# Kernel tuning notes

Measured on AMD Instinct MI355X. Metric: run time of the kernel, lower is better.

Reference implementation:

```python
import jax, jax.numpy as jnp
import numpy as np

B, TT, TA, H = 2, 128, 512, 1024
EPS = 1e-5


def _conv1d(x, w, b, pad):
    # x: [B, C_in, T], w: [C_out, C_in, K] -> [B, C_out, T]
    y = jax.lax.conv_general_dilated(x, w, window_strides=(1,), padding=[(pad, pad)],
                                     dimension_numbers=('NCH', 'OIH', 'NCH'))
    return y + b[None, :, None]


def _groupnorm1(x, g, b):
    # GroupNorm(num_groups=1): normalize over (C, T) per sample. x: [B, C, T]
    mu = jnp.mean(x, axis=(1, 2), keepdims=True)
    var = jnp.var(x, axis=(1, 2), keepdims=True)
    xn = (x - mu) * jax.lax.rsqrt(var + EPS)
    return xn * g[None, :, None] + b[None, :, None]


def setup_inputs() -> dict:
    key = jax.random.key(0)
    ks = jax.random.split(key, 16)
    s = 0.02
    return {
        'text_hidden': jax.random.normal(ks[0], (B, TT, H), jnp.float32),
        'audio_hidden': jax.random.normal(ks[1], (B, TA, H), jnp.float32),
        # alignment_proj: Linear(2H, H) -> ReLU -> Linear(H, 1)
        'a_w1': jax.random.normal(ks[2], (2 * H, H), jnp.float32) * s,
        'a_b1': jnp.zeros((H,), jnp.float32),
        'a_w2': jax.random.normal(ks[3], (H, 1), jnp.float32) * s,
        'a_b2': jnp.zeros((1,), jnp.float32),
        # duration_predictor: Conv1d(H,H,3) ReLU GN(1,H) Conv1d(H,H,3) ReLU GN(1,H) Conv1d(H,1,1)
        'd_w1': jax.random.normal(ks[4], (H, H, 3), jnp.float32) * s,
        'd_b1': jnp.zeros((H,), jnp.float32),
        'gn1_g': jnp.ones((H,), jnp.float32),
        'gn1_b': jnp.zeros((H,), jnp.float32),
        'd_w2': jax.random.normal(ks[5], (H, H, 3), jnp.float32) * s,
        'd_b2': jnp.zeros((H,), jnp.float32),
        'gn2_g': jnp.ones((H,), jnp.float32),
        'gn2_b': jnp.zeros((H,), jnp.float32),
        'd_w3': jax.random.normal(ks[6], (1, H, 1), jnp.float32) * s,
        'd_b3': jnp.zeros((1,), jnp.float32),
    }


def reference(text_hidden, audio_hidden, a_w1, a_b1, a_w2, a_b2,
              d_w1, d_b1, gn1_g, gn1_b, d_w2, d_b2, gn2_g, gn2_b, d_w3, d_b3):
    # ---- predict_durations ----
    x = jnp.swapaxes(text_hidden, 1, 2)                      # [B, H, TT]
    x = _groupnorm1(jax.nn.relu(_conv1d(x, d_w1, d_b1, 1)), gn1_g, gn1_b)
    x = _groupnorm1(jax.nn.relu(_conv1d(x, d_w2, d_b2, 1)), gn2_g, gn2_b)
    x = _conv1d(x, d_w3, d_b3, 0)                            # [B, 1, TT]
    durations = jax.nn.softplus(x[:, 0, :])                  # [B, TT]

    # ---- soft_mas (temperature = 1.0) ----
    # Linear on concat([text, audio]) == text @ W1[:H] + audio @ W1[H:] + b1
    t_part = jnp.einsum('bth,hd->btd', text_hidden, a_w1[:H])    # [B, TT, H]
    a_part = jnp.einsum('bah,hd->bad', audio_hidden, a_w1[H:])   # [B, TA, H]
    hid = jax.nn.relu(t_part[:, :, None, :] + a_part[:, None, :, :] + a_b1)  # [B,TT,TA,H]
    logits = jnp.einsum('btad,do->bta', hid, a_w2) + a_b2[0]     # [B, TT, TA]

    pos = jnp.arange(TA, dtype=logits.dtype)                     # audio positions j
    expected = jnp.arange(TT, dtype=logits.dtype) * (TA / TT)    # expected pos per text i
    monotonic_bias = -0.1 * jnp.abs(pos[None, :] - expected[:, None])  # [TT, TA]
    logits = logits + monotonic_bias[None, :, :]

    alignment = jax.nn.softmax(logits, axis=-1)
    return alignment, durations
```

## Files before the change

### kernel.cpp

```cpp
#include <hip/hip_runtime.h>
#include <hip/hip_bf16.h>


typedef __bf16 bf16_t;
typedef __bf16 bf16x8 __attribute__((ext_vector_type(8)));
typedef __bf16 bf16x4 __attribute__((ext_vector_type(4)));
typedef float  f32x4  __attribute__((ext_vector_type(4)));
typedef _Float16 f16_t;
typedef _Float16 f16x2 __attribute__((ext_vector_type(2)));
typedef _Float16 f16x4 __attribute__((ext_vector_type(4)));

#define EPSV 1e-5f

#define OFF_TEXTBF   0u
#define OFF_AUDIOBF  524288u
#define OFF_W1TOP    2621440u
#define OFF_W1BOT    4718592u
#define OFF_WC1      6815744u
#define OFF_WC2      13107200u
#define OFF_TP       19398656u
#define OFF_W2F      19922944u
#define OFF_APT      20447232u
#define OFF_XP0      22544384u
#define OFF_XP1      23076864u
#define OFF_Y2       23609344u
#define OFF_BST1     24133632u
#define OFF_BST2     24137728u
#define OFF_LP       24141824u
#define OFF_SG       26238976u
#define OFF_SB       26251264u
#define OFF_SGF      26263552u
#define OFF_SBF      26267648u

__global__ __launch_bounds__(256) void prep_k(
    const float* __restrict__ text, const float* __restrict__ audio,
    const float* __restrict__ w1,
    const float* __restrict__ w1c, const float* __restrict__ w2c,
    const float* __restrict__ w2,
    const float* __restrict__ g1, const float* __restrict__ b1g,
    bf16_t* __restrict__ text_bf, bf16_t* __restrict__ xp0,
    bf16_t* __restrict__ audio_bf,
    bf16_t* __restrict__ topT, bf16_t* __restrict__ botT,
    bf16_t* __restrict__ wc1, bf16_t* __restrict__ wc2,
    bf16_t* __restrict__ xp1, f16_t* __restrict__ w2f,
    float* __restrict__ Sg, float* __restrict__ Sb,
    float* __restrict__ SgF, float* __restrict__ SbF)
{
    __shared__ float tile[32][33];
    const int bid = blockIdx.x;
    if (bid < 1280) {
        const int e = (bid * 256 + threadIdx.x) * 4;
        if (e < 262144) {
            float4 v = *(const float4*)&text[e];
            bf16x4 o; o[0] = (bf16_t)v.x; o[1] = (bf16_t)v.y; o[2] = (bf16_t)v.z; o[3] = (bf16_t)v.w;
            *(bf16x4*)&text_bf[e] = o;
            const int bt = e >> 10, h = e & 1023;
            const int b = bt >> 7, t = bt & 127;
            *(bf16x4*)&xp0[(size_t)(b * 130 + 1 + t) * 1024 + h] = o;
        } else {
            const int ea = e - 262144;
            float4 v = *(const float4*)&audio[ea];
            bf16x4 o; o[0] = (bf16_t)v.x; o[1] = (bf16_t)v.y; o[2] = (bf16_t)v.z; o[3] = (bf16_t)v.w;
            *(bf16x4*)&audio_bf[ea] = o;
        }
    } else if (bid < 3328) {
        const int b2 = bid - 1280;
        const int bx = b2 & 31, by = b2 >> 5;
        const int tx = threadIdx.x & 31, ty = threadIdx.x >> 5;
        #pragma unroll
        for (int j = 0; j < 4; ++j)
            tile[ty + j * 8][tx] = w1[(size_t)(by * 32 + ty + j * 8) * 1024 + bx * 32 + tx];
        __syncthreads();
        bf16_t* out = (by < 32) ? topT : botT;
        const int hbase = (by & 31) * 32;
        #pragma unroll
        for (int j = 0; j < 4; ++j) {
            const int d = bx * 32 + ty + j * 8;
            out[(size_t)d * 1024 + hbase + tx] = (bf16_t)tile[tx][ty + j * 8];
        }
    } else if (bid < 5376) {
        int b2 = bid - 3328;
        const int is2 = (b2 >= 1024) ? 1 : 0;
        const float* w = is2 ? w2c : w1c;
        bf16_t* wc = is2 ? wc2 : wc1;
        b2 &= 1023;
        const int o = b2, i4 = threadIdx.x;
        const float* src = w + (size_t)o * 3072 + i4 * 12;
        float4 v0 = *(const float4*)&src[0];
        float4 v1 = *(const float4*)&src[4];
        float4 v2 = *(const float4*)&src[8];
        const float f[12] = {v0.x, v0.y, v0.z, v0.w, v1.x, v1.y, v1.z, v1.w, v2.x, v2.y, v2.z, v2.w};
        float g4[4] = {1.f, 1.f, 1.f, 1.f}, bb4[4] = {0.f, 0.f, 0.f, 0.f};
        if (is2) {
            float4 gv = *(const float4*)&g1[i4 * 4];
            float4 bv = *(const float4*)&b1g[i4 * 4];
            g4[0] = gv.x; g4[1] = gv.y; g4[2] = gv.z; g4[3] = gv.w;
            bb4[0] = bv.x; bb4[1] = bv.y; bb4[2] = bv.z; bb4[3] = bv.w;
        }
        float sgr[3] = {0.f, 0.f, 0.f}, sbr[3] = {0.f, 0.f, 0.f};
        #pragma unroll
        for (int r = 0; r < 3; ++r) {
            bf16x4 o4;
            #pragma unroll
            for (int j = 0; j < 4; ++j) {
                const float wv = f[j * 3 + r];
                const float ws = wv * g4[j];
                sgr[r] += ws;
                sbr[r] += wv * bb4[j];
                o4[j] = (bf16_t)(is2 ? ws : wv);
            }
            *(bf16x4*)&wc[(size_t)r * 1048576 + (size_t)o * 1024 + i4 * 4] = o4;
        }
        if (is2) {
            #pragma unroll
            for (int off = 32; off > 0; off >>= 1) {
                #pragma unroll
                for (int r = 0; r < 3; ++r) {
                    sgr[r] += __shfl_xor(sgr[r], off);
                    sbr[r] += __shfl_xor(sbr[r], off);
                }
            }
            float* red = &tile[0][0];
            const int wid = threadIdx.x >> 6, lane = threadIdx.x & 63;
            if (lane == 0) {
                #pragma unroll
                for (int r = 0; r < 3; ++r) {
                    red[wid * 6 + r] = sgr[r];
                    red[wid * 6 + 3 + r] = sbr[r];
                }
            }
            __syncthreads();
            if (threadIdx.x < 6) {
                const float v = red[threadIdx.x] + red[6 + threadIdx.x]
                              + red[12 + threadIdx.x] + red[18 + threadIdx.x];
                if (threadIdx.x < 3) Sg[o * 3 + threadIdx.x] = v;
                else                 Sb[o * 3 + threadIdx.x - 3] = v;
                red[24 + threadIdx.x] = v;
            }
            __syncthreads();
            if (threadIdx.x == 0)      SgF[o] = red[24] + red[25] + red[26];
            else if (threadIdx.x == 1) SbF[o] = red[27] + red[28] + red[29];
        }
    } else {
        const int tid = threadIdx.x;
        const int rowmap[4] = {0, 129, 130, 259};
        const int f = tid * 16;
        const int r = f >> 10, w = f & 1023;
        bf16x8 z8 = (bf16x8)(bf16_t)0.0f;
        bf16_t* p0 = xp0 + (size_t)rowmap[r] * 1024 + w;
        bf16_t* p1 = xp1 + (size_t)rowmap[r] * 1024 + w;
        *(bf16x8*)p0 = z8; *(bf16x8*)(p0 + 8) = z8;
        *(bf16x8*)p1 = z8; *(bf16x8*)(p1 + 8) = z8;
        float4 wv = *(const float4*)&w2[tid * 4];
        f16x4 wo; wo[0] = (f16_t)wv.x; wo[1] = (f16_t)wv.y; wo[2] = (f16_t)wv.z; wo[3] = (f16_t)wv.w;
        *(f16x4*)&w2f[tid * 4] = wo;
    }
}

__device__ __forceinline__ float wave_red_add(float v) {
    #pragma unroll
    for (int off = 32; off > 0; off >>= 1) v += __shfl_xor(v, off);
    return v;
}

__device__ __forceinline__ void conv_wave_partial(
    const bf16_t* __restrict__ Wc, const bf16_t* __restrict__ xp,
    int m0, int b, int tbase, int w, int l, f32x4& acc0, f32x4& acc1)
{
    const int lm = l & 15, lk = (l >> 4) * 8;
    const int koff = w * 128;
    const bf16_t* aq = Wc + (size_t)(m0 + lm) * 1024 + koff + lk;
    const bf16_t* bq = xp + (size_t)(b * 130 + tbase + lm) * 1024 + koff + lk;
    #pragma unroll
    for (int s = 0; s < 2; ++s) {
        bf16x8 ra[6], rb0[6], rb1[6];
        #pragma unroll
        for (int j = 0; j < 6; ++j) {
            const int idx = s * 6 + j;
            const int rr = idx >> 2, cc = idx & 3;
            const bf16_t* pa = aq + (size_t)rr * 1048576 + cc * 32;
            const bf16_t* pb = bq + (size_t)rr * 1024 + cc * 32;
            ra[j]  = *(const bf16x8*)pa;
            rb0[j] = *(const bf16x8*)pb;
            rb1[j] = *(const bf16x8*)(pb + 16384);
        }
        #pragma unroll
        for (int j = 0; j < 6; ++j) {
            acc0 = __builtin_amdgcn_mfma_f32_16x16x32_bf16(ra[j], rb0[j], acc0, 0, 0, 0);
            acc1 = __builtin_amdgcn_mfma_f32_16x16x32_bf16(ra[j], rb1[j], acc1, 0, 0, 0);
        }
    }
}

__global__ __launch_bounds__(512) void p2_k(
    const bf16_t* __restrict__ wc1, const bf16_t* __restrict__ xp0,
    const float* __restrict__ d_b1, bf16_t* __restrict__ xp1,
    float* __restrict__ bstat1,
    const bf16_t* __restrict__ text_bf, const bf16_t* __restrict__ w1topT,
    const float* __restrict__ a_b1, f16_t* __restrict__ tp,
    const bf16_t* __restrict__ audio_bf, const bf16_t* __restrict__ w1botT,
    f16_t* __restrict__ apT4)
{
    __shared__ float smem[8448];
    __shared__ float sred[8], sredq[8];
    const int bid = blockIdx.x;
    const int tid = threadIdx.x;
    const int w = tid >> 6, l = tid & 63;
    const int lm = l & 15, lh = l >> 4, lk = lh * 8;
    if (bid < 512) {
        const int bx = bid >> 6, by = bid & 63;
        const int bt0 = bx * 32, m0 = by * 16;
        const int b = bt0 >> 7, tbase = bt0 & 127;
        f32x4 acc0 = (f32x4)(0.0f), acc1 = (f32x4)(0.0f);
        conv_wave_partial(wc1, xp0, m0, b, tbase, w, l, acc0, acc1);
        float* sl = smem + w * 528;
        #pragma unroll
        for (int r = 0; r < 4; ++r) {
            sl[(lh * 4 + r) * 33 + lm] = acc0[r];
            sl[(lh * 4 + r) * 33 + 16 + lm] = acc1[r];
        }
        __syncthreads();
        const int mm = tid >> 5, nn = tid & 31;
        float v = 0.f;
        #pragma unroll
        for (int ww = 0; ww < 8; ++ww) v += smem[ww * 528 + mm * 33 + nn];
        v = fmaxf(v + d_b1[m0 + mm], 0.f);
        float s = wave_red_add(v), q = wave_red_add(v * v);
        if (l == 0) { sred[w] = s; sredq[w] = q; }
        xp1[(size_t)(b * 130 + 1 + tbase + nn) * 1024 + m0 + mm] = (bf16_t)v;
        __syncthreads();
        if (tid == 0) {
            float ts = 0.f, tq = 0.f;
            #pragma unroll
            for (int ww = 0; ww < 8; ++ww) { ts += sred[ww]; tq += sredq[ww]; }
            bstat1[bid * 2] = ts; bstat1[bid * 2 + 1] = tq;
        }
    } else {
        const bf16_t *At, *Bm;
        int d0, r0, is_tp;
        if (bid < 768) {
            const int unit = bid - 512;
            d0 = (unit & 31) * 32; r0 = (unit >> 5) * 32;
            At = w1topT; Bm = text_bf; is_tp = 1;
        } else {
            const int unit = bid - 768;
            d0 = (unit & 31) * 32; r0 = (unit >> 5) * 32;
            At = w1botT; Bm = audio_bf; is_tp = 0;
        }
        const int koff = w * 128;
        const bf16_t* Ap = At + (size_t)(d0 + lm) * 1024 + koff + lk;
        const bf16_t* Bp = Bm + (size_t)(r0 + lm) * 1024 + koff + lk;
        bf16x8 qa0[4], qa1[4], qb0[4], qb1[4];
        #pragma unroll
        for (int cc = 0; cc < 4; ++cc) {
            qa0[cc] = *(const bf16x8*)(Ap + cc * 32);
            qa1[cc] = *(const bf16x8*)(Ap + 16384 + cc * 32);
            qb0[cc] = *(const bf16x8*)(Bp + cc * 32);
            qb1[cc] = *(const bf16x8*)(Bp + 16384 + cc * 32);
        }
        f32x4 acc[2][2];
        #pragma unroll
        for (int mt = 0; mt < 2; ++mt)
            #pragma unroll
            for (int nt = 0; nt < 2; ++nt) acc[mt][nt] = (f32x4)(0.0f);
        #pragma unroll
        for (int cc = 0; cc < 4; ++cc) {
            acc[0][0] = __builtin_amdgcn_mfma_f32_16x16x32_bf16(qa0[cc], qb0[cc], acc[0][0], 0, 0, 0);
            acc[0][1] = __builtin_amdgcn_mfma_f32_16x16x32_bf16(qa0[cc], qb1[cc], acc[0][1], 0, 0, 0);
            acc[1][0] = __builtin_amdgcn_mfma_f32_16x16x32_bf16(qa1[cc], qb0[cc], acc[1][0], 0, 0, 0);
            acc[1][1] = __builtin_amdgcn_mfma_f32_16x16x32_bf16(qa1[cc], qb1[cc], acc[1][1], 0, 0, 0);
        }
        float* sl = smem + w * 1056;
        #pragma unroll
        for (int mt = 0; mt < 2; ++mt)
            #pragma unroll
            for (int nt = 0; nt < 2; ++nt)
                #pragma unroll
                for (int r = 0; r < 4; ++r)
                    sl[(mt * 16 + lh * 4 + r) * 33 + nt * 16 + lm] = acc[mt][nt][r];
        __syncthreads();
        const int m = tid >> 4, n2 = (tid & 15) * 2;
        float v0 = 0.f, v1 = 0.f;
        #pragma unroll
        for (int ww = 0; ww < 8; ++ww) {
            v0 += smem[ww * 1056 + m * 33 + n2];
            v1 += smem[ww * 1056 + m * 33 + n2 + 1];
        }
        if (is_tp) {
            const float bb = a_b1[d0 + m];
            tp[(size_t)(r0 + n2) * 1024 + d0 + m] = (f16_t)(v0 + bb);
            tp[(size_t)(r0 + n2 + 1) * 1024 + d0 + m] = (f16_t)(v1 + bb);
        } else {
            const int h = d0 + m, hq = h >> 2, hr = h & 3;
            const int a0 = r0 + n2;
            const int bbk = a0 >> 9, al = a0 & 511;
            apT4[((size_t)hq * 1024 + bbk * 512 + al) * 4 + hr] = (f16_t)v0;
            apT4[((size_t)hq * 1024 + bbk * 512 + al + 1) * 4 + hr] = (f16_t)v1;
        }
    }
}

__device__ __forceinline__ void reduce_bstat(
    const float* __restrict__ bstat, int b, int tid,
    float* sr, float* sq, float& mu, float& rsig)
{
    const int lane = tid & 63, wid = tid >> 6;
    float s = 0.f, q = 0.f;
    if (tid < 256) {
        float2 v = ((const float2*)bstat)[b * 256 + tid];
        s = v.x; q = v.y;
    }
    #pragma unroll
    for (int off = 32; off > 0; off >>= 1) {
        s += __shfl_xor(s, off);
        q += __shfl_xor(q, off);
    }
    if (lane == 0) { sr[wid] = s; sq[wid] = q; }
    __syncthreads();
    float ts = 0.f, tq = 0.f;
    #pragma unroll
    for (int i = 0; i < 8; ++i) { ts += sr[i]; tq += sq[i]; }
    const float cnt = 131072.f;
    mu = ts / cnt;
    const float var = tq / cnt - mu * mu;
    rsig = rsqrtf(var + EPSV);
}

__device__ __forceinline__ float dot2_acc(f16x2 x, f16x2 w, float acc) {
#if __has_builtin(__builtin_amdgcn_fdot2)
    return __builtin_amdgcn_fdot2(x, w, acc, false);
#else
    return acc + (float)x[0] * (float)w[0] + (float)x[1] * (float)w[1];
#endif
}

__global__ __launch_bounds__(512) void p3_k(
    const bf16_t* __restrict__ wc2, const bf16_t* __restrict__ xp1,
    const float* __restrict__ d_b2, bf16_t* __restrict__ y2,
    float* __restrict__ bstat2, const float* __restrict__ bstat1,
    const float* __restrict__ SgF, const float* __restrict__ SbF,
    const float* __restrict__ Sg3, const float* __restrict__ Sb3,
    const f16_t* __restrict__ tp, const f16_t* __restrict__ apT4,
    const f16_t* __restrict__ w2f, float* __restrict__ lp)
{
    __shared__ float smem[4224];
    __shared__ float sred[8], sredq[8], sr[8], sq[8];
    const int bid = blockIdx.x;
    const int tid = threadIdx.x;
    if (bid < 512) {
        const int w = tid >> 6, l = tid & 63;
        const int lm = l & 15, lh = l >> 4;
        const int bx = bid >> 6, by = bid & 63;
        const int bt0 = bx * 32, m0 = by * 16;
        const int b = bt0 >> 7, tbase = bt0 & 127;
        f32x4 acc0 = (f32x4)(0.0f), acc1 = (f32x4)(0.0f);
        conv_wave_partial(wc2, xp1, m0, b, tbase, w, l, acc0, acc1);
        float* sl = smem + w * 528;
        #pragma unroll
        for (int r = 0; r < 4; ++r) {
            sl[(lh * 4 + r) * 33 + lm] = acc0[r];
            sl[(lh * 4 + r) * 33 + 16 + lm] = acc1[r];
        }
        __syncthreads();
        const int mm = tid >> 5, nn = tid & 31;
        float vraw = 0.f;
        #pragma unroll
        for (int ww = 0; ww < 8; ++ww) vraw += smem[ww * 528 + mm * 33 + nn];
        float mu, rsig;
        reduce_bstat(bstat1, b, tid, sr, sq, mu, rsig);
        const int o = m0 + mm, tloc = tbase + nn;
        float sg = SgF[o], sb = SbF[o];
        if (tloc == 0)   { sg -= Sg3[o * 3];     sb -= Sb3[o * 3]; }
        if (tloc == 127) { sg -= Sg3[o * 3 + 2]; sb -= Sb3[o * 3 + 2]; }
        float v = fmaxf(rsig * vraw + sb - mu * rsig * sg + d_b2[o], 0.f);
        float s = wave_red_add(v), q = wave_red_add(v * v);
        if ((tid & 63) == 0) { sred[tid >> 6] = s; sredq[tid >> 6] = q; }
        y2[(size_t)(b * 128 + tloc) * 1024 + o] = (bf16_t)v;
        __syncthreads();
        if (tid == 0) {
            float ts = 0.f, tq = 0.f;
            #pragma unroll
            for (int ww = 0; ww < 8; ++ww) { ts += sred[ww]; tq += sredq[ww]; }
            bstat2[bid * 2] = ts; bstat2[bid * 2 + 1] = tq;
        }
    } else {
        const int lb = bid - 512;
        const int hc = lb >> 6, btp = lb & 63;
        const int bt0 = btp * 4;
        const int b = bt0 >> 7;
        const int a = tid;
        const f16_t* tpr = tp + (size_t)bt0 * 1024 + hc * 256;
        const f16_t* w2r = w2f + hc * 256;
        const f16_t* apc = apT4 + ((size_t)(hc * 64) * 1024 + b * 512 + a) * 4;
        float acc[4] = {0.f, 0.f, 0.f, 0.f};
        const f16x2 zero = (f16x2)(f16_t)0.0f;
#define L_A0(i) (*(const f16x4*)(apc + (size_t)(2 * (i)) * 4096))
#define L_A1(i) (*(const f16x4*)(apc + (size_t)(2 * (i) + 1) * 4096))
        constexpr int PF = 4;
        f16x4 pa[PF], pb[PF];
        #pragma unroll
        for (int i = 0; i < PF; ++i) { pa[i] = L_A0(i); pb[i] = L_A1(i); }
        #pragma unroll
        for (int i = 0; i < 32; ++i) {
            const int sl = i % PF;
            const int hq = 2 * i;
            f16x4 a0 = pa[sl], a1 = pb[sl];
            f16x4 w0 = *(const f16x4*)&w2r[hq * 4];
            f16x4 w1 = *(const f16x4*)&w2r[hq * 4 + 4];
            #pragma unroll
            for (int r = 0; r < 4; ++r) {
                f16x4 t0 = *(const f16x4*)&tpr[r * 1024 + hq * 4];
                f16x4 t1 = *(const f16x4*)&tpr[r * 1024 + hq * 4 + 4];
                f16x2 p;
                p = __builtin_elementwise_max((f16x2){t0[0] + a0[0], t0[1] + a0[1]}, zero);
                acc[r] = dot2_acc(p, (f16x2){w0[0], w0[1]}, acc[r]);
                p = __builtin_elementwise_max((f16x2){t0[2] + a0[2], t0[3] + a0[3]}, zero);
                acc[r] = dot2_acc(p, (f16x2){w0[2], w0[3]}, acc[r]);
                p = __builtin_elementwise_max((f16x2){t1[0] + a1[0], t1[1] + a1[1]}, zero);
                acc[r] = dot2_acc(p, (f16x2){w1[0], w1[1]}, acc[r]);
                p = __builtin_elementwise_max((f16x2){t1[2] + a1[2], t1[3] + a1[3]}, zero);
                acc[r] = dot2_acc(p, (f16x2){w1[2], w1[3]}, acc[r]);
            }
            const int nx = i + PF;
            if (nx < 32) { pa[sl] = L_A0(nx); pb[sl] = L_A1(nx); }
        }
#undef L_A0
#undef L_A1
        float* dst = lp + (size_t)(hc * 256 + bt0) * 512 + a;
        #pragma unroll
        for (int r = 0; r < 4; ++r) dst[(size_t)r * 512] = acc[r];
    }
}

__global__ __launch_bounds__(512) void combine_k(
    const float* __restrict__ lp, const float* __restrict__ b2,
    const bf16_t* __restrict__ y2, const float* __restrict__ bstat2,
    const float* __restrict__ g, const float* __restrict__ bet,
    const float* __restrict__ w3, const float* __restrict__ b3,
    float* __restrict__ out)
{
    __shared__ float redm[8], redsum[8];
    const int bid = blockIdx.x;
    const int tid = threadIdx.x;
    if (bid < 256) {
        const int bt = bid, t = bt & 127;
        const int a = tid;
        const int lane = a & 63, wid = a >> 6;
        const size_t base = (size_t)bt * 512 + a;
        float v = lp[base] + lp[131072 + base] + lp[262144 + base] + lp[393216 + base];
        v += b2[0] - 0.1f * fabsf((float)a - 4.0f * (float)t);
        float m = v;
        #pragma unroll
        for (int off = 32; off > 0; off >>= 1) m = fmaxf(m, __shfl_xor(m, off));
        if (lane == 0) redm[wid] = m;
        __syncthreads();
        float M = redm[0];
        #pragma unroll
        for (int i = 1; i < 8; ++i) M = fmaxf(M, redm[i]);
        const float e = expf(v - M);
        float s = e;
        #pragma unroll
        for (int off = 32; off > 0; off >>= 1) s += __shfl_xor(s, off);
        if (lane == 0) redsum[wid] = s;
        __syncthreads();
        float S = redsum[0];
        #pragma unroll
        for (int i = 1; i < 8; ++i) S += redsum[i];
        out[(size_t)bt * 512 + a] = e * (1.0f / S);
    } else {
        const int cb = bid - 256;
        const int b = (cb * 8) >> 7;
        float mu, rsig;
        reduce_bstat(bstat2, b, tid, redm, redsum, mu, rsig);
        const int lane = tid & 63, w = tid >> 6;
        const int bt = cb * 8 + w;
        const bf16_t* row = y2 + (size_t)bt * 1024 + lane * 16;
        float s1 = 0.f, s2 = 0.f, s3 = 0.f;
        #pragma unroll
        for (int c = 0; c < 2; ++c) {
            bf16x8 yv = *(const bf16x8*)(row + c * 8);
            #pragma unroll
            for (int j = 0; j < 8; ++j) {
                const int i = lane * 16 + c * 8 + j;
                const float gw = g[i] * w3[i];
                s1 += gw * (float)yv[j];
                s2 += gw;
                s3 += bet[i] * w3[i];
            }
        }
        #pragma unroll
        for (int off = 32; off > 0; off >>= 1) {
            s1 += __shfl_xor(s1, off);
            s2 += __shfl_xor(s2, off);
            s3 += __shfl_xor(s3, off);
        }
        if (lane == 0) {
            const float t = rsig * (s1 - mu * s2) + s3 + b3[0];
            out[131072 + bt] = fmaxf(t, 0.f) + log1pf(expf(-fabsf(t)));
        }
    }
}

extern "C" void kernel_launch(void* const* d_in, const int* in_sizes, int n_in,
                              void* d_out, int out_size, void* d_ws, size_t ws_size,
                              hipStream_t stream) {
    const float* text   = (const float*)d_in[0];
    const float* audio  = (const float*)d_in[1];
    const float* a_w1   = (const float*)d_in[2];
    const float* a_b1   = (const float*)d_in[3];
    const float* a_w2   = (const float*)d_in[4];
    const float* a_b2   = (const float*)d_in[5];
    const float* d_w1   = (const float*)d_in[6];
    const float* d_b1   = (const float*)d_in[7];
    const float* gn1_g  = (const float*)d_in[8];
    const float* gn1_b  = (const float*)d_in[9];
    const float* d_w2   = (const float*)d_in[10];
    const float* d_b2   = (const float*)d_in[11];
    const float* gn2_g  = (const float*)d_in[12];
    const float* gn2_b  = (const float*)d_in[13];
    const float* d_w3   = (const float*)d_in[14];
    const float* d_b3   = (const float*)d_in[15];

    char* ws = (char*)d_ws;
    float* outf = (float*)d_out;

    bf16_t* text_bf  = (bf16_t*)(ws + OFF_TEXTBF);
    bf16_t* audio_bf = (bf16_t*)(ws + OFF_AUDIOBF);
    bf16_t* w1topT   = (bf16_t*)(ws + OFF_W1TOP);
    bf16_t* w1botT   = (bf16_t*)(ws + OFF_W1BOT);
    bf16_t* wc1      = (bf16_t*)(ws + OFF_WC1);
    bf16_t* wc2      = (bf16_t*)(ws + OFF_WC2);
    f16_t*  tp       = (f16_t*) (ws + OFF_TP);
    f16_t*  w2f      = (f16_t*) (ws + OFF_W2F);
    f16_t*  apT4     = (f16_t*) (ws + OFF_APT);
    bf16_t* xp0      = (bf16_t*)(ws + OFF_XP0);
    bf16_t* xp1      = (bf16_t*)(ws + OFF_XP1);
    bf16_t* y2       = (bf16_t*)(ws + OFF_Y2);
    float*  bstat1   = (float*) (ws + OFF_BST1);
    float*  bstat2   = (float*) (ws + OFF_BST2);
    float*  lp       = (float*) (ws + OFF_LP);
    float*  Sg3     = (float*) (ws + OFF_SG);
    float*  Sb3     = (float*) (ws + OFF_SB);
    float*  SgFp    = (float*) (ws + OFF_SGF);
    float*  SbFp    = (float*) (ws + OFF_SBF);

    prep_k<<<dim3(5377), 256, 0, stream>>>(text, audio, a_w1, d_w1, d_w2, a_w2,
                                           gn1_g, gn1_b,
                                           text_bf, xp0, audio_bf, w1topT, w1botT,
                                           wc1, wc2, xp1, w2f, Sg3, Sb3,
                                           SgFp, SbFp);
    p2_k<<<dim3(1792), 512, 0, stream>>>(wc1, xp0, d_b1, xp1, bstat1,
                                         text_bf, w1topT, a_b1, tp,
                                         audio_bf, w1botT, apT4);
    p3_k<<<dim3(768), 512, 0, stream>>>(wc2, xp1, d_b2, y2, bstat2, bstat1,
                                        SgFp, SbFp, Sg3, Sb3, tp, apT4, w2f, lp);
    combine_k<<<dim3(288), 512, 0, stream>>>(lp, a_b2, y2, bstat2,
                                             gn2_g, gn2_b, d_w3, d_b3, outf);
}
```

Before: 179.5 us.

## Fuse four phase kernels into one cooperative persistent kernel with grid syncs

Turns the four separate kernel launches (prep, phase A, phase B, combine) into one cooperative kernel with 256 persistent blocks. The blocks loop over work units and use grid-wide barriers between phases. This aims to remove launch gaps and tail drain between kernels. In exchange it caps parallelism at 256 blocks, with each block running many units in sequence, and adds grid sync costs. A fallback to separate launches is kept in case the cooperative launch fails.

After: 294.8 us. +64.2%, slower.

```diff
diff --git a/kernel.cpp b/kernel.cpp
--- a/kernel.cpp
+++ b/kernel.cpp
@@ -1,5 +1,8 @@
 #include <hip/hip_runtime.h>
 #include <hip/hip_bf16.h>
+#include <hip/hip_cooperative_groups.h>
+
+namespace cg = cooperative_groups;
 
 
 typedef __bf16 bf16_t;
@@ -32,130 +35,14 @@
 #define OFF_SGF      26263552u
 #define OFF_SBF      26267648u
 
-__global__ __launch_bounds__(256) void prep_k(
-    const float* __restrict__ text, const float* __restrict__ audio,
-    const float* __restrict__ w1,
-    const float* __restrict__ w1c, const float* __restrict__ w2c,
-    const float* __restrict__ w2,
-    const float* __restrict__ g1, const float* __restrict__ b1g,
-    bf16_t* __restrict__ text_bf, bf16_t* __restrict__ xp0,
-    bf16_t* __restrict__ audio_bf,
-    bf16_t* __restrict__ topT, bf16_t* __restrict__ botT,
-    bf16_t* __restrict__ wc1, bf16_t* __restrict__ wc2,
-    bf16_t* __restrict__ xp1, f16_t* __restrict__ w2f,
-    float* __restrict__ Sg, float* __restrict__ Sb,
-    float* __restrict__ SgF, float* __restrict__ SbF)
-{
-    __shared__ float tile[32][33];
-    const int bid = blockIdx.x;
-    if (bid < 1280) {
-        const int e = (bid * 256 + threadIdx.x) * 4;
-        if (e < 262144) {
-            float4 v = *(const float4*)&text[e];
-            bf16x4 o; o[0] = (bf16_t)v.x; o[1] = (bf16_t)v.y; o[2] = (bf16_t)v.z; o[3] = (bf16_t)v.w;
-            *(bf16x4*)&text_bf[e] = o;
-            const int bt = e >> 10, h = e & 1023;
-            const int b = bt >> 7, t = bt & 127;
-            *(bf16x4*)&xp0[(size_t)(b * 130 + 1 + t) * 1024 + h] = o;
-        } else {
-            const int ea = e - 262144;
-            float4 v = *(const float4*)&audio[ea];
-            bf16x4 o; o[0] = (bf16_t)v.x; o[1] = (bf16_t)v.y; o[2] = (bf16_t)v.z; o[3] = (bf16_t)v.w;
-            *(bf16x4*)&audio_bf[ea] = o;
-        }
-    } else if (bid < 3328) {
-        const int b2 = bid - 1280;
-        const int bx = b2 & 31, by = b2 >> 5;
-        const int tx = threadIdx.x & 31, ty = threadIdx.x >> 5;
-        #pragma unroll
-        for (int j = 0; j < 4; ++j)
-            tile[ty + j * 8][tx] = w1[(size_t)(by * 32 + ty + j * 8) * 1024 + bx * 32 + tx];
-        __syncthreads();
-        bf16_t* out = (by < 32) ? topT : botT;
-        const int hbase = (by & 31) * 32;
-        #pragma unroll
-        for (int j = 0; j < 4; ++j) {
-            const int d = bx * 32 + ty + j * 8;
-            out[(size_t)d * 1024 + hbase + tx] = (bf16_t)tile[tx][ty + j * 8];
-        }
-    } else if (bid < 5376) {
-        int b2 = bid - 3328;
-        const int is2 = (b2 >= 1024) ? 1 : 0;
-        const float* w = is2 ? w2c : w1c;
-        bf16_t* wc = is2 ? wc2 : wc1;
-        b2 &= 1023;
-        const int o = b2, i4 = threadIdx.x;
-        const float* src = w + (size_t)o * 3072 + i4 * 12;
-        float4 v0 = *(const float4*)&src[0];
-        float4 v1 = *(const float4*)&src[4];
-        float4 v2 = *(const float4*)&src[8];
-        const float f[12] = {v0.x, v0.y, v0.z, v0.w, v1.x, v1.y, v1.z, v1.w, v2.x, v2.y, v2.z, v2.w};
-        float g4[4] = {1.f, 1.f, 1.f, 1.f}, bb4[4] = {0.f, 0.f, 0.f, 0.f};
-        if (is2) {
-            float4 gv = *(const float4*)&g1[i4 * 4];
-            float4 bv = *(const float4*)&b1g[i4 * 4];
-            g4[0] = gv.x; g4[1] = gv.y; g4[2] = gv.z; g4[3] = gv.w;
-            bb4[0] = bv.x; bb4[1] = bv.y; bb4[2] = bv.z; bb4[3] = bv.w;
-        }
-        float sgr[3] = {0.f, 0.f, 0.f}, sbr[3] = {0.f, 0.f, 0.f};
-        #pragma unroll
-        for (int r = 0; r < 3; ++r) {
-            bf16x4 o4;
-            #pragma unroll
-            for (int j = 0; j < 4; ++j) {
-                const float wv = f[j * 3 + r];
-                const float ws = wv * g4[j];
-                sgr[r] += ws;
-                sbr[r] += wv * bb4[j];
-                o4[j] = (bf16_t)(is2 ? ws : wv);
-            }
-            *(bf16x4*)&wc[(size_t)r * 1048576 + (size_t)o * 1024 + i4 * 4] = o4;
-        }
-        if (is2) {
-            #pragma unroll
-            for (int off = 32; off > 0; off >>= 1) {
-                #pragma unroll
-                for (int r = 0; r < 3; ++r) {
-                    sgr[r] += __shfl_xor(sgr[r], off);
-                    sbr[r] += __shfl_xor(sbr[r], off);
-                }
-            }
-            float* red = &tile[0][0];
-            const int wid = threadIdx.x >> 6, lane = threadIdx.x & 63;
-            if (lane == 0) {
-                #pragma unroll
-                for (int r = 0; r < 3; ++r) {
-                    red[wid * 6 + r] = sgr[r];
-                    red[wid * 6 + 3 + r] = sbr[r];
-                }
-            }
-            __syncthreads();
-            if (threadIdx.x < 6) {
-                const float v = red[threadIdx.x] + red[6 + threadIdx.x]
-                              + red[12 + threadIdx.x] + red[18 + threadIdx.x];
-                if (threadIdx.x < 3) Sg[o * 3 + threadIdx.x] = v;
-                else                 Sb[o * 3 + threadIdx.x - 3] = v;
-                red[24 + threadIdx.x] = v;
-            }
-            __syncthreads();
-            if (threadIdx.x == 0)      SgF[o] = red[24] + red[25] + red[26];
-            else if (threadIdx.x == 1) SbF[o] = red[27] + red[28] + red[29];
-        }
-    } else {
-        const int tid = threadIdx.x;
-        const int rowmap[4] = {0, 129, 130, 259};
-        const int f = tid * 16;
-        const int r = f >> 10, w = f & 1023;
-        bf16x8 z8 = (bf16x8)(bf16_t)0.0f;
-        bf16_t* p0 = xp0 + (size_t)rowmap[r] * 1024 + w;
-        bf16_t* p1 = xp1 + (size_t)rowmap[r] * 1024 + w;
-        *(bf16x8*)p0 = z8; *(bf16x8*)(p0 + 8) = z8;
-        *(bf16x8*)p1 = z8; *(bf16x8*)(p1 + 8) = z8;
-        float4 wv = *(const float4*)&w2[tid * 4];
-        f16x4 wo; wo[0] = (f16_t)wv.x; wo[1] = (f16_t)wv.y; wo[2] = (f16_t)wv.z; wo[3] = (f16_t)wv.w;
-        *(f16x4*)&w2f[tid * 4] = wo;
-    }
-}
+struct KP {
+    const float *text, *audio, *w1, *w1c, *w2c, *w2raw, *g1, *b1g;
+    const float *db1, *ab1, *db2, *ab2, *g2, *bet2, *w3, *b3;
+    bf16_t *text_bf, *audio_bf, *topT, *botT, *wc1, *wc2, *xp0, *xp1, *y2;
+    f16_t *tp, *w2f, *apT4;
+    float *bstat1, *bstat2, *lp, *Sg3, *Sb3, *SgF, *SbF;
+    float *out;
+};
 
 __device__ __forceinline__ float wave_red_add(float v) {
     #pragma unroll
@@ -188,114 +75,6 @@
         for (int j = 0; j < 6; ++j) {
             acc0 = __builtin_amdgcn_mfma_f32_16x16x32_bf16(ra[j], rb0[j], acc0, 0, 0, 0);
             acc1 = __builtin_amdgcn_mfma_f32_16x16x32_bf16(ra[j], rb1[j], acc1, 0, 0, 0);
-        }
-    }
-}
-
-__global__ __launch_bounds__(512) void p2_k(
-    const bf16_t* __restrict__ wc1, const bf16_t* __restrict__ xp0,
-    const float* __restrict__ d_b1, bf16_t* __restrict__ xp1,
-    float* __restrict__ bstat1,
-    const bf16_t* __restrict__ text_bf, const bf16_t* __restrict__ w1topT,
-    const float* __restrict__ a_b1, f16_t* __restrict__ tp,
-    const bf16_t* __restrict__ audio_bf, const bf16_t* __restrict__ w1botT,
-    f16_t* __restrict__ apT4)
-{
-    __shared__ float smem[8448];
-    __shared__ float sred[8], sredq[8];
-    const int bid = blockIdx.x;
-    const int tid = threadIdx.x;
-    const int w = tid >> 6, l = tid & 63;
-    const int lm = l & 15, lh = l >> 4, lk = lh * 8;
-    if (bid < 512) {
-        const int bx = bid >> 6, by = bid & 63;
-        const int bt0 = bx * 32, m0 = by * 16;
-        const int b = bt0 >> 7, tbase = bt0 & 127;
-        f32x4 acc0 = (f32x4)(0.0f), acc1 = (f32x4)(0.0f);
-        conv_wave_partial(wc1, xp0, m0, b, tbase, w, l, acc0, acc1);
-        float* sl = smem + w * 528;
-        #pragma unroll
-        for (int r = 0; r < 4; ++r) {
-            sl[(lh * 4 + r) * 33 + lm] = acc0[r];
-            sl[(lh * 4 + r) * 33 + 16 + lm] = acc1[r];
-        }
-        __syncthreads();
-        const int mm = tid >> 5, nn = tid & 31;
-        float v = 0.f;
-        #pragma unroll
-        for (int ww = 0; ww < 8; ++ww) v += smem[ww * 528 + mm * 33 + nn];
-        v = fmaxf(v + d_b1[m0 + mm], 0.f);
-        float s = wave_red_add(v), q = wave_red_add(v * v);
-        if (l == 0) { sred[w] = s; sredq[w] = q; }
-        xp1[(size_t)(b * 130 + 1 + tbase + nn) * 1024 + m0 + mm] = (bf16_t)v;
-        __syncthreads();
-        if (tid == 0) {
-            float ts = 0.f, tq = 0.f;
-            #pragma unroll
-            for (int ww = 0; ww < 8; ++ww) { ts += sred[ww]; tq += sredq[ww]; }
-            bstat1[bid * 2] = ts; bstat1[bid * 2 + 1] = tq;
-        }
-    } else {
-        const bf16_t *At, *Bm;
-        int d0, r0, is_tp;
-        if (bid < 768) {
-            const int unit = bid - 512;
-            d0 = (unit & 31) * 32; r0 = (unit >> 5) * 32;
-            At = w1topT; Bm = text_bf; is_tp = 1;
-        } else {
-            const int unit = bid - 768;
-            d0 = (unit & 31) * 32; r0 = (unit >> 5) * 32;
-            At = w1botT; Bm = audio_bf; is_tp = 0;
-        }
-        const int koff = w * 128;
-        const bf16_t* Ap = At + (size_t)(d0 + lm) * 1024 + koff + lk;
-        const bf16_t* Bp = Bm + (size_t)(r0 + lm) * 1024 + koff + lk;
-        bf16x8 qa0[4], qa1[4], qb0[4], qb1[4];
-        #pragma unroll
-        for (int cc = 0; cc < 4; ++cc) {
-            qa0[cc] = *(const bf16x8*)(Ap + cc * 32);
-            qa1[cc] = *(const bf16x8*)(Ap + 16384 + cc * 32);
-            qb0[cc] = *(const bf16x8*)(Bp + cc * 32);
-            qb1[cc] = *(const bf16x8*)(Bp + 16384 + cc * 32);
-        }
-        f32x4 acc[2][2];
-        #pragma unroll
-        for (int mt = 0; mt < 2; ++mt)
-            #pragma unroll
-            for (int nt = 0; nt < 2; ++nt) acc[mt][nt] = (f32x4)(0.0f);
-        #pragma unroll
-        for (int cc = 0; cc < 4; ++cc) {
-            acc[0][0] = __builtin_amdgcn_mfma_f32_16x16x32_bf16(qa0[cc], qb0[cc], acc[0][0], 0, 0, 0);
-            acc[0][1] = __builtin_amdgcn_mfma_f32_16x16x32_bf16(qa0[cc], qb1[cc], acc[0][1], 0, 0, 0);
-            acc[1][0] = __builtin_amdgcn_mfma_f32_16x16x32_bf16(qa1[cc], qb0[cc], acc[1][0], 0, 0, 0);
-            acc[1][1] = __builtin_amdgcn_mfma_f32_16x16x32_bf16(qa1[cc], qb1[cc], acc[1][1], 0, 0, 0);
-        }
-        float* sl = smem + w * 1056;
-        #pragma unroll
-        for (int mt = 0; mt < 2; ++mt)
-            #pragma unroll
-            for (int nt = 0; nt < 2; ++nt)
-                #pragma unroll
-                for (int r = 0; r < 4; ++r)
-                    sl[(mt * 16 + lh * 4 + r) * 33 + nt * 16 + lm] = acc[mt][nt][r];
-        __syncthreads();
-        const int m = tid >> 4, n2 = (tid & 15) * 2;
-        float v0 = 0.f, v1 = 0.f;
-        #pragma unroll
-        for (int ww = 0; ww < 8; ++ww) {
-            v0 += smem[ww * 1056 + m * 33 + n2];
-            v1 += smem[ww * 1056 + m * 33 + n2 + 1];
-        }
-        if (is_tp) {
-            const float bb = a_b1[d0 + m];
-            tp[(size_t)(r0 + n2) * 1024 + d0 + m] = (f16_t)(v0 + bb);
-            tp[(size_t)(r0 + n2 + 1) * 1024 + d0 + m] = (f16_t)(v1 + bb);
-        } else {
-            const int h = d0 + m, hq = h >> 2, hr = h & 3;
-            const int a0 = r0 + n2;
-            const int bbk = a0 >> 9, al = a0 & 511;
-            apT4[((size_t)hq * 1024 + bbk * 512 + al) * 4 + hr] = (f16_t)v0;
-            apT4[((size_t)hq * 1024 + bbk * 512 + al + 1) * 4 + hr] = (f16_t)v1;
         }
     }
 }
@@ -334,27 +113,126 @@
 #endif
 }
 
-__global__ __launch_bounds__(512) void p3_k(
-    const bf16_t* __restrict__ wc2, const bf16_t* __restrict__ xp1,
-    const float* __restrict__ d_b2, bf16_t* __restrict__ y2,
-    float* __restrict__ bstat2, const float* __restrict__ bstat1,
-    const float* __restrict__ SgF, const float* __restrict__ SbF,
-    const float* __restrict__ Sg3, const float* __restrict__ Sb3,
-    const f16_t* __restrict__ tp, const f16_t* __restrict__ apT4,
-    const f16_t* __restrict__ w2f, float* __restrict__ lp)
-{
-    __shared__ float smem[4224];
-    __shared__ float sred[8], sredq[8], sr[8], sq[8];
-    const int bid = blockIdx.x;
-    const int tid = threadIdx.x;
-    if (bid < 512) {
-        const int w = tid >> 6, l = tid & 63;
-        const int lm = l & 15, lh = l >> 4;
-        const int bx = bid >> 6, by = bid & 63;
+__device__ void prep_unit(int u, int t, float* tile, const KP& p)
+{
+    if (u < 1280) {
+        const int e = (u * 256 + t) * 4;
+        if (e < 262144) {
+            float4 v = *(const float4*)&p.text[e];
+            bf16x4 o; o[0] = (bf16_t)v.x; o[1] = (bf16_t)v.y; o[2] = (bf16_t)v.z; o[3] = (bf16_t)v.w;
+            *(bf16x4*)&p.text_bf[e] = o;
+            const int bt = e >> 10, h = e & 1023;
+            const int b = bt >> 7, tt = bt & 127;
+            *(bf16x4*)&p.xp0[(size_t)(b * 130 + 1 + tt) * 1024 + h] = o;
+        } else {
+            const int ea = e - 262144;
+            float4 v = *(const float4*)&p.audio[ea];
+            bf16x4 o; o[0] = (bf16_t)v.x; o[1] = (bf16_t)v.y; o[2] = (bf16_t)v.z; o[3] = (bf16_t)v.w;
+            *(bf16x4*)&p.audio_bf[ea] = o;
+        }
+    } else if (u < 3328) {
+        const int b2 = u - 1280;
+        const int bx = b2 & 31, by = b2 >> 5;
+        const int tx = t & 31, ty = t >> 5;
+        #pragma unroll
+        for (int j = 0; j < 4; ++j)
+            tile[(ty + j * 8) * 33 + tx] = p.w1[(size_t)(by * 32 + ty + j * 8) * 1024 + bx * 32 + tx];
+        __syncthreads();
+        bf16_t* out = (by < 32) ? p.topT : p.botT;
+        const int hbase = (by & 31) * 32;
+        #pragma unroll
+        for (int j = 0; j < 4; ++j) {
+            const int d = bx * 32 + ty + j * 8;
+            out[(size_t)d * 1024 + hbase + tx] = (bf16_t)tile[tx * 33 + ty + j * 8];
+        }
+    } else if (u < 5376) {
+        int b2 = u - 3328;
+        const int is2 = (b2 >= 1024) ? 1 : 0;
+        const float* wsrc = is2 ? p.w2c : p.w1c;
+        bf16_t* wc = is2 ? p.wc2 : p.wc1;
+        b2 &= 1023;
+        const int o = b2, i4 = t;
+        const float* src = wsrc + (size_t)o * 3072 + i4 * 12;
+        float4 v0 = *(const float4*)&src[0];
+        float4 v1 = *(const float4*)&src[4];
+        float4 v2 = *(const float4*)&src[8];
+        const float f[12] = {v0.x, v0.y, v0.z, v0.w, v1.x, v1.y, v1.z, v1.w, v2.x, v2.y, v2.z, v2.w};
+        float g4[4] = {1.f, 1.f, 1.f, 1.f}, bb4[4] = {0.f, 0.f, 0.f, 0.f};
+        if (is2) {
+            float4 gv = *(const float4*)&p.g1[i4 * 4];
+            float4 bv = *(const float4*)&p.b1g[i4 * 4];
+            g4[0] = gv.x; g4[1] = gv.y; g4[2] = gv.z; g4[3] = gv.w;
+            bb4[0] = bv.x; bb4[1] = bv.y; bb4[2] = bv.z; bb4[3] = bv.w;
+        }
+        float sgr[3] = {0.f, 0.f, 0.f}, sbr[3] = {0.f, 0.f, 0.f};
+        #pragma unroll
+        for (int r = 0; r < 3; ++r) {
+            bf16x4 o4;
+            #pragma unroll
+            for (int j = 0; j < 4; ++j) {
+                const float wv = f[j * 3 + r];
+                const float ws = wv * g4[j];
+                sgr[r] += ws;
+                sbr[r] += wv * bb4[j];
+                o4[j] = (bf16_t)(is2 ? ws : wv);
+            }
+            *(bf16x4*)&wc[(size_t)r * 1048576 + (size_t)o * 1024 + i4 * 4] = o4;
+        }
+        if (is2) {
+            #pragma unroll
+            for (int off = 32; off > 0; off >>= 1) {
+                #pragma unroll
+                for (int r = 0; r < 3; ++r) {
+                    sgr[r] += __shfl_xor(sgr[r], off);
+                    sbr[r] += __shfl_xor(sbr[r], off);
+                }
+            }
+            float* red = tile;
+            const int wid = t >> 6, lane = t & 63;
+            if (lane == 0) {
+                #pragma unroll
+                for (int r = 0; r < 3; ++r) {
+                    red[wid * 6 + r] = sgr[r];
+                    red[wid * 6 + 3 + r] = sbr[r];
+                }
+            }
+            __syncthreads();
+            if (t < 6) {
+                const float v = red[t] + red[6 + t] + red[12 + t] + red[18 + t];
+                if (t < 3) p.Sg3[o * 3 + t] = v;
+                else       p.Sb3[o * 3 + t - 3] = v;
+                red[24 + t] = v;
+            }
+            __syncthreads();
+            if (t == 0)      p.SgF[o] = red[24] + red[25] + red[26];
+            else if (t == 1) p.SbF[o] = red[27] + red[28] + red[29];
+        }
+    } else {
+        const int rowmap[4] = {0, 129, 130, 259};
+        const int f = t * 16;
+        const int r = f >> 10, ww = f & 1023;
+        bf16x8 z8 = (bf16x8)(bf16_t)0.0f;
+        bf16_t* p0 = p.xp0 + (size_t)rowmap[r] * 1024 + ww;
+        bf16_t* p1 = p.xp1 + (size_t)rowmap[r] * 1024 + ww;
+        *(bf16x8*)p0 = z8; *(bf16x8*)(p0 + 8) = z8;
+        *(bf16x8*)p1 = z8; *(bf16x8*)(p1 + 8) = z8;
+        float4 wv = *(const float4*)&p.w2raw[t * 4];
+        f16x4 wo; wo[0] = (f16_t)wv.x; wo[1] = (f16_t)wv.y; wo[2] = (f16_t)wv.z; wo[3] = (f16_t)wv.w;
+        *(f16x4*)&p.w2f[t * 4] = wo;
+    }
+}
+
+__device__ void phaseA_unit(int u, int tid, float* smem,
+                            float* sred, float* sredq, const KP& p)
+{
+    const int w = tid >> 6, l = tid & 63;
+    const int lm = l & 15, lh = l >> 4, lk = lh * 8;
+    if (u < 512) {
+        const int bx = u >> 6, by = u & 63;
         const int bt0 = bx * 32, m0 = by * 16;
         const int b = bt0 >> 7, tbase = bt0 & 127;
         f32x4 acc0 = (f32x4)(0.0f), acc1 = (f32x4)(0.0f);
-        conv_wave_partial(wc2, xp1, m0, b, tbase, w, l, acc0, acc1);
+        conv_wave_partial(p.wc1, p.xp0, m0, b, tbase, w, l, acc0, acc1);
         float* sl = smem + w * 528;
         #pragma unroll
         for (int r = 0; r < 4; ++r) {
@@ -363,35 +241,135 @@
         }
         __syncthreads();
         const int mm = tid >> 5, nn = tid & 31;
+        float v = 0.f;
+        #pragma unroll
+        for (int ww = 0; ww < 8; ++ww) v += smem[ww * 528 + mm * 33 + nn];
+        v = fmaxf(v + p.db1[m0 + mm], 0.f);
+        float s = wave_red_add(v), q = wave_red_add(v * v);
+        if (l == 0) { sred[w] = s; sredq[w] = q; }
+        p.xp1[(size_t)(b * 130 + 1 + tbase + nn) * 1024 + m0 + mm] = (bf16_t)v;
+        __syncthreads();
+        if (tid == 0) {
+            float ts = 0.f, tq = 0.f;
+            #pragma unroll
+            for (int ww = 0; ww < 8; ++ww) { ts += sred[ww]; tq += sredq[ww]; }
+            p.bstat1[u * 2] = ts; p.bstat1[u * 2 + 1] = tq;
+        }
+    } else {
+        const int is_tp = (u < 768) ? 1 : 0;
+        int d0, r0;
+        const bf16_t *At, *Bm;
+        if (is_tp) {
+            const int un = u - 512;
+            d0 = (un & 31) * 32; r0 = (un >> 5) * 32;
+            At = p.topT; Bm = p.text_bf;
+        } else {
+            const int un = u - 768;
+            d0 = (un & 31) * 32; r0 = (un >> 5) * 32;
+            At = p.botT; Bm = p.audio_bf;
+        }
+        const int koff = w * 128;
+        const bf16_t* Ap = At + (size_t)(d0 + lm) * 1024 + koff + lk;
+        const bf16_t* Bp = Bm + (size_t)(r0 + lm) * 1024 + koff + lk;
+        bf16x8 qa0[4], qa1[4], qb0[4], qb1[4];
+        #pragma unroll
+        for (int cc = 0; cc < 4; ++cc) {
+            qa0[cc] = *(const bf16x8*)(Ap + cc * 32);
+            qa1[cc] = *(const bf16x8*)(Ap + 16384 + cc * 32);
+            qb0[cc] = *(const bf16x8*)(Bp + cc * 32);
+            qb1[cc] = *(const bf16x8*)(Bp + 16384 + cc * 32);
+        }
+        f32x4 acc[2][2];
+        #pragma unroll
+        for (int mt = 0; mt < 2; ++mt)
+            #pragma unroll
+            for (int nt = 0; nt < 2; ++nt) acc[mt][nt] = (f32x4)(0.0f);
+        #pragma unroll
+        for (int cc = 0; cc < 4; ++cc) {
+            acc[0][0] = __builtin_amdgcn_mfma_f32_16x16x32_bf16(qa0[cc], qb0[cc], acc[0][0], 0, 0, 0);
+            acc[0][1] = __builtin_amdgcn_mfma_f32_16x16x32_bf16(qa0[cc], qb1[cc], acc[0][1], 0, 0, 0);
+            acc[1][0] = __builtin_amdgcn_mfma_f32_16x16x32_bf16(qa1[cc], qb0[cc], acc[1][0], 0, 0, 0);
+            acc[1][1] = __builtin_amdgcn_mfma_f32_16x16x32_bf16(qa1[cc], qb1[cc], acc[1][1], 0, 0, 0);
+        }
+        float* sl = smem + w * 1056;
+        #pragma unroll
+        for (int mt = 0; mt < 2; ++mt)
+            #pragma unroll
+            for (int nt = 0; nt < 2; ++nt)
+                #pragma unroll
+                for (int r = 0; r < 4; ++r)
+                    sl[(mt * 16 + lh * 4 + r) * 33 + nt * 16 + lm] = acc[mt][nt][r];
+        __syncthreads();
+        const int m = tid >> 4, n2 = (tid & 15) * 2;
+        float v0 = 0.f, v1 = 0.f;
+        #pragma unroll
+        for (int ww = 0; ww < 8; ++ww) {
+            v0 += smem[ww * 1056 + m * 33 + n2];
+            v1 += smem[ww * 1056 + m * 33 + n2 + 1];
+        }
+        if (is_tp) {
+            const float bb = p.ab1[d0 + m];
+            p.tp[(size_t)(r0 + n2) * 1024 + d0 + m] = (f16_t)(v0 + bb);
+            p.tp[(size_t)(r0 + n2 + 1) * 1024 + d0 + m] = (f16_t)(v1 + bb);
+        } else {
+            const int h = d0 + m, hq = h >> 2, hr = h & 3;
+            const int a0 = r0 + n2;
+            const int bbk = a0 >> 9, al = a0 & 511;
+            p.apT4[((size_t)hq * 1024 + bbk * 512 + al) * 4 + hr] = (f16_t)v0;
+            p.apT4[((size_t)hq * 1024 + bbk * 512 + al + 1) * 4 + hr] = (f16_t)v1;
+        }
+    }
+}
+
+__device__ void phaseB_unit(int u, int tid, float* smem,
+                            float* sred, float* sredq, float* sr8, float* sq8,
+                            const KP& p)
+{
+    if (u < 512) {
+        const int w = tid >> 6, l = tid & 63;
+        const int lm = l & 15, lh = l >> 4;
+        const int bx = u >> 6, by = u & 63;
+        const int bt0 = bx * 32, m0 = by * 16;
+        const int b = bt0 >> 7, tbase = bt0 & 127;
+        f32x4 acc0 = (f32x4)(0.0f), acc1 = (f32x4)(0.0f);
+        conv_wave_partial(p.wc2, p.xp1, m0, b, tbase, w, l, acc0, acc1);
+        float* sl = smem + w * 528;
+        #pragma unroll
+        for (int r = 0; r < 4; ++r) {
+            sl[(lh * 4 + r) * 33 + lm] = acc0[r];
+            sl[(lh * 4 + r) * 33 + 16 + lm] = acc1[r];
+        }
+        __syncthreads();
+        const int mm = tid >> 5, nn = tid & 31;
         float vraw = 0.f;
         #pragma unroll
         for (int ww = 0; ww < 8; ++ww) vraw += smem[ww * 528 + mm * 33 + nn];
         float mu, rsig;
-        reduce_bstat(bstat1, b, tid, sr, sq, mu, rsig);
+        reduce_bstat(p.bstat1, b, tid, sr8, sq8, mu, rsig);
         const int o = m0 + mm, tloc = tbase + nn;
-        float sg = SgF[o], sb = SbF[o];
-        if (tloc == 0)   { sg -= Sg3[o * 3];     sb -= Sb3[o * 3]; }
-        if (tloc == 127) { sg -= Sg3[o * 3 + 2]; sb -= Sb3[o * 3 + 2]; }
-        float v = fmaxf(rsig * vraw + sb - mu * rsig * sg + d_b2[o], 0.f);
+        float sg = p.SgF[o], sb = p.SbF[o];
+        if (tloc == 0)   { sg -= p.Sg3[o * 3];     sb -= p.Sb3[o * 3]; }
+        if (tloc == 127) { sg -= p.Sg3[o * 3 + 2]; sb -= p.Sb3[o * 3 + 2]; }
+        float v = fmaxf(rsig * vraw + sb - mu * rsig * sg + p.db2[o], 0.f);
         float s = wave_red_add(v), q = wave_red_add(v * v);
         if ((tid & 63) == 0) { sred[tid >> 6] = s; sredq[tid >> 6] = q; }
-        y2[(size_t)(b * 128 + tloc) * 1024 + o] = (bf16_t)v;
+        p.y2[(size_t)(b * 128 + tloc) * 1024 + o] = (bf16_t)v;
         __syncthreads();
         if (tid == 0) {
             float ts = 0.f, tq = 0.f;
             #pragma unroll
             for (int ww = 0; ww < 8; ++ww) { ts += sred[ww]; tq += sredq[ww]; }
-            bstat2[bid * 2] = ts; bstat2[bid * 2 + 1] = tq;
+            p.bstat2[u * 2] = ts; p.bstat2[u * 2 + 1] = tq;
         }
     } else {
-        const int lb = bid - 512;
+        const int lb = u - 512;
         const int hc = lb >> 6, btp = lb & 63;
         const int bt0 = btp * 4;
         const int b = bt0 >> 7;
         const int a = tid;
-        const f16_t* tpr = tp + (size_t)bt0 * 1024 + hc * 256;
-        const f16_t* w2r = w2f + hc * 256;
-        const f16_t* apc = apT4 + ((size_t)(hc * 64) * 1024 + b * 512 + a) * 4;
+        const f16_t* tpr = p.tp + (size_t)bt0 * 1024 + hc * 256;
+        const f16_t* w2r = p.w2f + hc * 256;
+        const f16_t* apc = p.apT4 + ((size_t)(hc * 64) * 1024 + b * 512 + a) * 4;
         float acc[4] = {0.f, 0.f, 0.f, 0.f};
         const f16x2 zero = (f16x2)(f16_t)0.0f;
 #define L_A0(i) (*(const f16x4*)(apc + (size_t)(2 * (i)) * 4096))
@@ -411,70 +389,64 @@
             for (int r = 0; r < 4; ++r) {
                 f16x4 t0 = *(const f16x4*)&tpr[r * 1024 + hq * 4];
                 f16x4 t1 = *(const f16x4*)&tpr[r * 1024 + hq * 4 + 4];
-                f16x2 p;
-                p = __builtin_elementwise_max((f16x2){t0[0] + a0[0], t0[1] + a0[1]}, zero);
-                acc[r] = dot2_acc(p, (f16x2){w0[0], w0[1]}, acc[r]);
-                p = __builtin_elementwise_max((f16x2){t0[2] + a0[2], t0[3] + a0[3]}, zero);
-                acc[r] = dot2_acc(p, (f16x2){w0[2], w0[3]}, acc[r]);
-                p = __builtin_elementwise_max((f16x2){t1[0] + a1[0], t1[1] + a1[1]}, zero);
-                acc[r] = dot2_acc(p, (f16x2){w1[0], w1[1]}, acc[r]);
-                p = __builtin_elementwise_max((f16x2){t1[2] + a1[2], t1[3] + a1[3]}, zero);
-                acc[r] = dot2_acc(p, (f16x2){w1[2], w1[3]}, acc[r]);
+                f16x2 pp;
+                pp = __builtin_elementwise_max((f16x2){t0[0] + a0[0], t0[1] + a0[1]}, zero);
+                acc[r] = dot2_acc(pp, (f16x2){w0[0], w0[1]}, acc[r]);
+                pp = __builtin_elementwise_max((f16x2){t0[2] + a0[2], t0[3] + a0[3]}, zero);
+                acc[r] = dot2_acc(pp, (f16x2){w0[2], w0[3]}, acc[r]);
+                pp = __builtin_elementwise_max((f16x2){t1[0] + a1[0], t1[1] + a1[1]}, zero);
+                acc[r] = dot2_acc(pp, (f16x2){w1[0], w1[1]}, acc[r]);
+                pp = __builtin_elementwise_max((f16x2){t1[2] + a1[2], t1[3] + a1[3]}, zero);
+                acc[r] = dot2_acc(pp, (f16x2){w1[2], w1[3]}, acc[r]);
             }
             const int nx = i + PF;
             if (nx < 32) { pa[sl] = L_A0(nx); pb[sl] = L_A1(nx); }
         }
 #undef L_A0
 #undef L_A1
-        float* dst = lp + (size_t)(hc * 256 + bt0) * 512 + a;
+        float* dst = p.lp + (size_t)(hc * 256 + bt0) * 512 + a;
         #pragma unroll
         for (int r = 0; r < 4; ++r) dst[(size_t)r * 512] = acc[r];
     }
 }
 
-__global__ __launch_bounds__(512) void combine_k(
-    const float* __restrict__ lp, const float* __restrict__ b2,
-    const bf16_t* __restrict__ y2, const float* __restrict__ bstat2,
-    const float* __restrict__ g, const float* __restrict__ bet,
-    const float* __restrict__ w3, const float* __restrict__ b3,
-    float* __restrict__ out)
-{
-    __shared__ float redm[8], redsum[8];
-    const int bid = blockIdx.x;
-    const int tid = threadIdx.x;
-    if (bid < 256) {
-        const int bt = bid, t = bt & 127;
+__device__ void phaseC_unit(int u, int tid,
+                            float* sred, float* sredq, float* sr8, float* sq8,
+                            const KP& p)
+{
+    if (u < 256) {
+        const int bt = u, t = bt & 127;
         const int a = tid;
         const int lane = a & 63, wid = a >> 6;
         const size_t base = (size_t)bt * 512 + a;
-        float v = lp[base] + lp[131072 + base] + lp[262144 + base] + lp[393216 + base];
-        v += b2[0] - 0.1f * fabsf((float)a - 4.0f * (float)t);
+        float v = p.lp[base] + p.lp[131072 + base] + p.lp[262144 + base] + p.lp[393216 + base];
+        v += p.ab2[0] - 0.1f * fabsf((float)a - 4.0f * (float)t);
         float m = v;
         #pragma unroll
         for (int off = 32; off > 0; off >>= 1) m = fmaxf(m, __shfl_xor(m, off));
-        if (lane == 0) redm[wid] = m;
-        __syncthreads();
-        float M = redm[0];
-        #pragma unroll
-        for (int i = 1; i < 8; ++i) M = fmaxf(M, redm[i]);
+        if (lane == 0) sred[wid] = m;
+        __syncthreads();
+        float M = sred[0];
+        #pragma unroll
+        for (int i = 1; i < 8; ++i) M = fmaxf(M, sred[i]);
         const float e = expf(v - M);
         float s = e;
         #pragma unroll
         for (int off = 32; off > 0; off >>= 1) s += __shfl_xor(s, off);
-        if (lane == 0) redsum[wid] = s;
-        __syncthreads();
-        float S = redsum[0];
-        #pragma unroll
-        for (int i = 1; i < 8; ++i) S += redsum[i];
-        out[(size_t)bt * 512 + a] = e * (1.0f / S);
+        if (lane == 0) sredq[wid] = s;
+        __syncthreads();
+        float S = sredq[0];
+        #pragma unroll
+        for (int i = 1; i < 8; ++i) S += sredq[i];
+        p.out[(size_t)bt * 512 + a] = e * (1.0f / S);
     } else {
-        const int cb = bid - 256;
+        const int cb = u - 256;
         const int b = (cb * 8) >> 7;
         float mu, rsig;
-        reduce_bstat(bstat2, b, tid, redm, redsum, mu, rsig);
-        const int lane = tid & 63, w = tid >> 6;
-        const int bt = cb * 8 + w;
-        const bf16_t* row = y2 + (size_t)bt * 1024 + lane * 16;
+        reduce_bstat(p.bstat2, b, tid, sr8, sq8, mu, rsig);
+        const int lane = tid & 63, ww = tid >> 6;
+        const int bt = cb * 8 + ww;
+        const bf16_t* row = p.y2 + (size_t)bt * 1024 + lane * 16;
         float s1 = 0.f, s2 = 0.f, s3 = 0.f;
         #pragma unroll
         for (int c = 0; c < 2; ++c) {
@@ -482,10 +454,10 @@
             #pragma unroll
             for (int j = 0; j < 8; ++j) {
                 const int i = lane * 16 + c * 8 + j;
-                const float gw = g[i] * w3[i];
+                const float gw = p.g2[i] * p.w3[i];
                 s1 += gw * (float)yv[j];
                 s2 += gw;
-                s3 += bet[i] * w3[i];
+                s3 += p.bet2[i] * p.w3[i];
             }
         }
         #pragma unroll
@@ -495,65 +467,109 @@
             s3 += __shfl_xor(s3, off);
         }
         if (lane == 0) {
-            const float t = rsig * (s1 - mu * s2) + s3 + b3[0];
-            out[131072 + bt] = fmaxf(t, 0.f) + log1pf(expf(-fabsf(t)));
-        }
-    }
+            const float t = rsig * (s1 - mu * s2) + s3 + p.b3[0];
+            p.out[131072 + bt] = fmaxf(t, 0.f) + log1pf(expf(-fabsf(t)));
+        }
+    }
+}
+
+__global__ __launch_bounds__(512, 2) void fused_k(KP p)
+{
+    cg::grid_group gg = cg::this_grid();
+    __shared__ float smem[8448];
+    __shared__ float sred[8], sredq[8], sr8[8], sq8[8];
+    const int gs = gridDim.x;
+    const int bid = blockIdx.x;
+    const int tid = threadIdx.x;
+
+    {
+        const int half = tid >> 8, t = tid & 255;
+        float* tile = smem + half * 1056;
+        for (int i = bid; i < 2689; i += gs) {
+            __syncthreads();
+            const int u = i * 2 + half;
+            if (u < 5377) prep_unit(u, t, tile, p);
+        }
+    }
+    gg.sync();
+    for (int u = bid; u < 1792; u += gs) { __syncthreads(); phaseA_unit(u, tid, smem, sred, sredq, p); }
+    gg.sync();
+    for (int u = bid; u < 768; u += gs) { __syncthreads(); phaseB_unit(u, tid, smem, sred, sredq, sr8, sq8, p); }
+    gg.sync();
+    for (int u = bid; u < 288; u += gs) { __syncthreads(); phaseC_unit(u, tid, sred, sredq, sr8, sq8, p); }
+}
+
+__global__ __launch_bounds__(256) void prep_sep(KP p) {
+    __shared__ float tile[1056];
+    prep_unit(blockIdx.x, threadIdx.x, tile, p);
+}
+__global__ __launch_bounds__(512) void pA_sep(KP p) {
+    __shared__ float smem[8448];
+    __shared__ float sred[8], sredq[8];
+    phaseA_unit(blockIdx.x, threadIdx.x, smem, sred, sredq, p);
+}
+__global__ __launch_bounds__(512) void pB_sep(KP p) {
+    __shared__ float smem[8448];
+    __shared__ float sred[8], sredq[8], sr8[8], sq8[8];
+    phaseB_unit(blockIdx.x, threadIdx.x, smem, sred, sredq, sr8, sq8, p);
+}
+__global__ __launch_bounds__(512) void pC_sep(KP p) {
+    __shared__ float sred[8], sredq[8], sr8[8], sq8[8];
+    phaseC_unit(blockIdx.x, threadIdx.x, sred, sredq, sr8, sq8, p);
 }
 
 extern "C" void kernel_launch(void* const* d_in, const int* in_sizes, int n_in,
                               void* d_out, int out_size, void* d_ws, size_t ws_size,
                               hipStream_t stream) {
-    const float* text   = (const float*)d_in[0];
-    const float* audio  = (const float*)d_in[1];
-    const float* a_w1   = (const float*)d_in[2];
-    const float* a_b1   = (const float*)d_in[3];
-    const float* a_w2   = (const float*)d_in[4];
-    const float* a_b2   = (const float*)d_in[5];
-    const float* d_w1   = (const float*)d_in[6];
-    const float* d_b1   = (const float*)d_in[7];
-    const float* gn1_g  = (const float*)d_in[8];
-    const float* gn1_b  = (const float*)d_in[9];
-    const float* d_w2   = (const float*)d_in[10];
-    const float* d_b2   = (const float*)d_in[11];
-    const float* gn2_g  = (const float*)d_in[12];
-    const float* gn2_b  = (const float*)d_in[13];
-    const float* d_w3   = (const float*)d_in[14];
-    const float* d_b3   = (const float*)d_in[15];
-
     char* ws = (char*)d_ws;
-    float* outf = (float*)d_out;
-
-    bf16_t* text_bf  = (bf16_t*)(ws + OFF_TEXTBF);
-    bf16_t* audio_bf = (bf16_t*)(ws + OFF_AUDIOBF);
-    bf16_t* w1topT   = (bf16_t*)(ws + OFF_W1TOP);
-    bf16_t* w1botT   = (bf16_t*)(ws + OFF_W1BOT);
-    bf16_t* wc1      = (bf16_t*)(ws + OFF_WC1);
-    bf16_t* wc2      = (bf16_t*)(ws + OFF_WC2);
-    f16_t*  tp       = (f16_t*) (ws + OFF_TP);
-    f16_t*  w2f      = (f16_t*) (ws + OFF_W2F);
-    f16_t*  apT4     = (f16_t*) (ws + OFF_APT);
-    bf16_t* xp0      = (bf16_t*)(ws + OFF_XP0);
-    bf16_t* xp1      = (bf16_t*)(ws + OFF_XP1);
-    bf16_t* y2       = (bf16_t*)(ws + OFF_Y2);
-    float*  bstat1   = (float*) (ws + OFF_BST1);
-    float*  bstat2   = (float*) (ws + OFF_BST2);
-    float*  lp       = (float*) (ws + OFF_LP);
-    float*  Sg3     = (float*) (ws + OFF_SG);
-    float*  Sb3     = (float*) (ws + OFF_SB);
-    float*  SgFp    = (float*) (ws + OFF_SGF);
-    float*  SbFp    = (float*) (ws + OFF_SBF);
-
-    prep_k<<<dim3(5377), 256, 0, stream>>>(text, audio, a_w1, d_w1, d_w2, a_w2,
-                                           gn1_g, gn1_b,
-                                           text_bf, xp0, audio_bf, w1topT, w1botT,
-                                           wc1, wc2, xp1, w2f, Sg3, Sb3,
-                                           SgFp, SbFp);
-    p2_k<<<dim3(1792), 512, 0, stream>>>(wc1, xp0, d_b1, xp1, bstat1,
-                                         text_bf, w1topT, a_b1, tp,
-                                         audio_bf, w1botT, apT4);
-    p3_k<<<dim3(768), 512, 0, stream>>>(wc2, xp1, d_b2, y2, bstat2, bstat1,
-                                        SgFp, SbFp, Sg3, Sb3, tp, apT4, w2f, lp);
-    combine_k<<<dim3(288), 512, 0, stream>>>(lp, a_b2, y2, bstat2,
-                                             gn2_g, gn2_b, d_w3, d_b3, outf);
-}
+
+    KP kp;
+    kp.text   = (const float*)d_in[0];
+    kp.audio  = (const float*)d_in[1];
+    kp.w1     = (const float*)d_in[2];
+    kp.ab1    = (const float*)d_in[3];
+    kp.w2raw  = (const float*)d_in[4];
+    kp.ab2    = (const float*)d_in[5];
+    kp.w1c    = (const float*)d_in[6];
+    kp.db1    = (const float*)d_in[7];
+    kp.g1     = (const float*)d_in[8];
+    kp.b1g    = (const float*)d_in[9];
+    kp.w2c    = (const float*)d_in[10];
+    kp.db2    = (const float*)d_in[11];
+    kp.g2     = (const float*)d_in[12];
+    kp.bet2   = (const float*)d_in[13];
+    kp.w3     = (const float*)d_in[14];
+    kp.b3     = (const float*)d_in[15];
+
+    kp.text_bf  = (bf16_t*)(ws + OFF_TEXTBF);
+    kp.audio_bf = (bf16_t*)(ws + OFF_AUDIOBF);
+    kp.topT     = (bf16_t*)(ws + OFF_W1TOP);
+    kp.botT     = (bf16_t*)(ws + OFF_W1BOT);
+    kp.wc1      = (bf16_t*)(ws + OFF_WC1);
+    kp.wc2      = (bf16_t*)(ws + OFF_WC2);
+    kp.tp       = (f16_t*) (ws + OFF_TP);
+    kp.w2f      = (f16_t*) (ws + OFF_W2F);
+    kp.apT4     = (f16_t*) (ws + OFF_APT);
+    kp.xp0      = (bf16_t*)(ws + OFF_XP0);
+    kp.xp1      = (bf16_t*)(ws + OFF_XP1);
+    kp.y2       = (bf16_t*)(ws + OFF_Y2);
+    kp.bstat1   = (float*) (ws + OFF_BST1);
+    kp.bstat2   = (float*) (ws + OFF_BST2);
+    kp.lp       = (float*) (ws + OFF_LP);
+    kp.Sg3      = (float*) (ws + OFF_SG);
+    kp.Sb3      = (float*) (ws + OFF_SB);
+    kp.SgF      = (float*) (ws + OFF_SGF);
+    kp.SbF      = (float*) (ws + OFF_SBF);
+    kp.out      = (float*)d_out;
+
+    void* args[] = { (void*)&kp };
+    hipError_t err = hipLaunchCooperativeKernel((void*)fused_k, dim3(256),
+                                                dim3(512), args, 0, stream);
+    if (err != hipSuccess) {
+        (void)hipGetLastError();
+        prep_sep<<<dim3(5377), 256, 0, stream>>>(kp);
+        pA_sep<<<dim3(1792), 512, 0, stream>>>(kp);
+        pB_sep<<<dim3(768), 512, 0, stream>>>(kp);
+        pC_sep<<<dim3(288), 512, 0, stream>>>(kp);
+    }
+}
```
